# Kernel optimization log

Measured on AMD Instinct MI355X. Metric: run time of the kernel, lower is better.

The kernel has to match this reference:

```python
import jax, jax.numpy as jnp
import numpy as np

B, S, D, H, T, MAXLEN = 8, 1024, 768, 12, 384, 1024
HD = D // H  # spatial head dim = 64
SCALE = HD ** -0.5


def setup_inputs() -> dict:
    key = jax.random.key(0)
    ks = jax.random.split(key, 16)

    def lin(k, din, dout):
        kw, _ = jax.random.split(k)
        w = jax.random.normal(kw, (din, dout), jnp.float32) / np.sqrt(din).astype(np.float32)
        b = jnp.zeros((dout,), jnp.float32)
        return w, b

    Wqs, bqs = lin(ks[0], D, D)
    Wks, bks = lin(ks[1], D, D)
    Wvs, bvs = lin(ks[2], D, D)
    Wqt, bqt = lin(ks[3], T, D)
    Wkt, bkt = lin(ks[4], T, D)
    Wvt, bvt = lin(ks[5], T, D)
    Er = jax.random.normal(ks[6], (MAXLEN, HD), jnp.float32)
    patches = jax.random.normal(ks[7], (B, S, D), jnp.float32)
    time_emb = jax.random.normal(ks[8], (B, T), jnp.float32)
    return dict(patches=patches, time_emb=time_emb,
                Wqs=Wqs, bqs=bqs, Wks=Wks, bks=bks, Wvs=Wvs, bvs=bvs,
                Wqt=Wqt, bqt=bqt, Wkt=Wkt, bkt=bkt, Wvt=Wvt, bvt=bvt, Er=Er)


def _skew(QEr):
    # QEr: [B, H, S, S] -> pad one zero col on the left, reshape, drop first row.
    b, h, r, c = QEr.shape
    padded = jnp.pad(QEr, ((0, 0), (0, 0), (0, 0), (1, 0)))  # [B,H,r,c+1]
    reshaped = padded.reshape(b, h, c + 1, r)
    return reshaped[:, :, 1:, :]  # [B,H,S,S]


def reference(patches, time_emb, Wqs, bqs, Wks, bks, Wvs, bvs,
              Wqt, bqt, Wkt, bkt, Wvt, bvt, Er):
    b, s, _ = patches.shape

    def heads(x):  # [B,S,D] -> [B,H,S,HD]
        return x.reshape(b, -1, H, HD).transpose(0, 2, 1, 3)

    qs = heads(patches @ Wqs + bqs)
    ks = heads(patches @ Wks + bks)
    vs = heads(patches @ Wvs + bvs)
    qt = heads(time_emb @ Wqt + bqt)  # [B,H,1,HD]
    kt = heads(time_emb @ Wkt + bkt)
    vt = heads(time_emb @ Wvt + bvt)

    q = qs + qt
    k = ks + kt
    v = vs + vt

    Er_slice = Er[MAXLEN - s:, :]                      # [S, HD]
    QEr = jnp.einsum('bhsd,td->bhst', qs, Er_slice)    # [B,H,S,S]
    Srel = _skew(QEr)

    scores = (jnp.einsum('bhqd,bhkd->bhqk', q, k) + Srel) * SCALE
    attn = jax.nn.softmax(scores, axis=-1)
    out = jnp.einsum('bhqk,bhkd->bhqd', attn, v)       # [B,H,S,HD]
    return out.transpose(0, 2, 1, 3).reshape(b, s, H * HD)
```

## Files before the change

kernel.cpp:

```cpp
#include <hip/hip_runtime.h>

typedef __attribute__((ext_vector_type(8))) short short8;
typedef __attribute__((ext_vector_type(4))) float floatx4;

#define CSC 0.1803368801f

__device__ __forceinline__ unsigned short f2b(float f){
  unsigned int u = __builtin_bit_cast(unsigned int, f);
  unsigned int r = (u + 0x7fffu + ((u >> 16) & 1u)) >> 16;
  return (unsigned short)r;
}
__device__ __forceinline__ float b2f(unsigned short h){
  unsigned int u = ((unsigned int)h) << 16;
  return __builtin_bit_cast(float, u);
}
__device__ __forceinline__ floatx4 mfma16(short8 a, short8 b, floatx4 c){
  return __builtin_amdgcn_mfma_f32_16x16x32_bf16(a, b, c, 0, 0, 0);
}

__global__ __launch_bounds__(256) void transpose_w(
    const float* __restrict__ Wq, const float* __restrict__ Wk,
    const float* __restrict__ Wv, unsigned short* __restrict__ Wb){
  __shared__ float tile[64][65];
  int g = blockIdx.z;
  const float* W = (g==0) ? Wq : (g==1) ? Wk : Wv;
  int r0 = blockIdx.y*64, c0 = blockIdx.x*64;
  int tx = threadIdx.x & 63, ty = threadIdx.x >> 6;
  #pragma unroll
  for (int i=0;i<16;i++){
    int r = i*4 + ty;
    tile[r][tx] = W[(r0+r)*768 + c0 + tx];
  }
  __syncthreads();
  unsigned short* dst = Wb + g*589824;
  #pragma unroll
  for (int i=0;i<16;i++){
    int rr = i*4 + ty;
    dst[(c0+rr)*768 + r0 + tx] = f2b(tile[tx][rr]);
  }
}

__global__ __launch_bounds__(256) void convert_kernel(
    const float* __restrict__ patches, const float* __restrict__ Er,
    const float* __restrict__ temb,
    const float* __restrict__ Wqt, const float* __restrict__ bqt,
    const float* __restrict__ Wkt, const float* __restrict__ bkt,
    const float* __restrict__ Wvt, const float* __restrict__ bvt,
    unsigned short* __restrict__ Pb, unsigned short* __restrict__ Erb,
    float* __restrict__ Tmat){
  int blk = blockIdx.x, tid = threadIdx.x;
  if (blk < 3104){
    const float* src; unsigned short* dst; int idx;
    if (blk < 3072){ idx = blk*2048 + tid*8; src = patches; dst = Pb; }
    else           { idx = (blk-3072)*2048 + tid*8; src = Er; dst = Erb; }
    float4 f0 = *(const float4*)(src + idx);
    float4 f1 = *(const float4*)(src + idx + 4);
    uint4 pk;
    pk.x = (unsigned)f2b(f0.x) | ((unsigned)f2b(f0.y)<<16);
    pk.y = (unsigned)f2b(f0.z) | ((unsigned)f2b(f0.w)<<16);
    pk.z = (unsigned)f2b(f1.x) | ((unsigned)f2b(f1.y)<<16);
    pk.w = (unsigned)f2b(f1.z) | ((unsigned)f2b(f1.w)<<16);
    *(uint4*)(dst + idx) = pk;
  } else {
    int g = (blk-3104)>>3, bb = (blk-3104)&7;
    const float* Wt = (g==0)? Wqt : (g==1)? Wkt : Wvt;
    const float* bt = (g==0)? bqt : (g==1)? bkt : bvt;
    __shared__ float emb[384];
    for (int j=tid;j<384;j+=256) emb[j] = temb[bb*384 + j];
    __syncthreads();
    float acc0 = bt[tid], acc1 = bt[tid+256], acc2 = bt[tid+512];
    for (int t=0;t<384;t++){
      float e = emb[t];
      const float* wr = Wt + t*768;
      acc0 += e*wr[tid]; acc1 += e*wr[tid+256]; acc2 += e*wr[tid+512];
    }
    float* dst = Tmat + g*6144 + bb*768;
    float s = (g==0) ? CSC : 1.0f;
    dst[tid] = acc0*s; dst[tid+256] = acc1*s; dst[tid+512] = acc2*s;
  }
}

__global__ __launch_bounds__(256) void qkv_gemm(
    const unsigned short* __restrict__ Pb, const unsigned short* __restrict__ Wb,
    const float* __restrict__ bq, const float* __restrict__ bk,
    const float* __restrict__ bv, const float* __restrict__ Tmat,
    unsigned short* __restrict__ Qs, unsigned short* __restrict__ K,
    unsigned short* __restrict__ V){
  __shared__ unsigned short a_lds[128*72];
  __shared__ unsigned short b_lds[128*72];
  int g = blockIdx.z;
  int m0 = blockIdx.x*128, n0 = blockIdx.y*128;
  int tid = threadIdx.x, w = tid>>6, lane = tid&63, quad = lane>>4, l16 = lane&15;
  int wr = w>>1, wc = w&1;
  const unsigned short* Wg = Wb + g*589824;
  const float* bias = (g==0)? bq : (g==1)? bk : bv;
  floatx4 acc[4][4];
  #pragma unroll
  for (int i=0;i<4;i++)
    #pragma unroll
    for (int j=0;j<4;j++) acc[i][j] = (floatx4){0.f,0.f,0.f,0.f};

  for (int kt=0; kt<12; kt++){
    int k0 = kt*64;
    __syncthreads();
    #pragma unroll
    for (int i=0;i<4;i++){
      int idx = i*256 + tid;
      int r = idx >> 3, c = (idx & 7) << 3;
      *(uint4*)&a_lds[r*72 + c] = *(const uint4*)&Pb[(m0+r)*768 + k0 + c];
      *(uint4*)&b_lds[r*72 + c] = *(const uint4*)&Wg[(n0+r)*768 + k0 + c];
    }
    __syncthreads();
    #pragma unroll
    for (int ks=0; ks<2; ks++){
      short8 af[4], bf[4];
      #pragma unroll
      for (int mb=0;mb<4;mb++)
        af[mb] = *(const short8*)&a_lds[(wr*64+mb*16+l16)*72 + ks*32 + quad*8];
      #pragma unroll
      for (int nb=0;nb<4;nb++)
        bf[nb] = *(const short8*)&b_lds[(wc*64+nb*16+l16)*72 + ks*32 + quad*8];
      #pragma unroll
      for (int mb=0;mb<4;mb++)
        #pragma unroll
        for (int nb=0;nb<4;nb++)
          acc[mb][nb] = mfma16(af[mb], bf[nb], acc[mb][nb]);
    }
  }
  #pragma unroll
  for (int mb=0;mb<4;mb++)
  #pragma unroll
  for (int nb=0;nb<4;nb++)
  #pragma unroll
  for (int reg=0;reg<4;reg++){
    int m = m0 + wr*64 + mb*16 + quad*4 + reg;
    int n = n0 + wc*64 + nb*16 + l16;
    int bb = m >> 10, s = m & 1023, h = n >> 6, hd = n & 63;
    float v = acc[mb][nb][reg] + bias[n];
    int base = (bb*12 + h) << 16;
    if (g == 0){
      Qs[base + (s<<6) + hd] = f2b(v * CSC);
    } else {
      float tadd = Tmat[g*6144 + bb*768 + n];
      if (g == 1) K[base + (s<<6) + hd] = f2b(v + tadd);
      else        V[base + (hd<<10) + s] = f2b(v + tadd);
    }
  }
}

__global__ __launch_bounds__(256, 4) void attn_kernel(
    const unsigned short* __restrict__ Qsp, const unsigned short* __restrict__ Kp,
    const unsigned short* __restrict__ Vtp, const unsigned short* __restrict__ Erb,
    const float* __restrict__ Tq, float* __restrict__ out){
  __shared__ __align__(16) char smem[29696];
  unsigned short* k_lds  = (unsigned short*)smem;
  unsigned short* v_lds  = (unsigned short*)(smem + 9216);
  unsigned short* pw_all = (unsigned short*)(smem + 18432);

  int tid = threadIdx.x, w = tid>>6, lane = tid&63, quad = lane>>4, l16 = lane&15;
  unsigned short* pw = pw_all + w*1408;
  int q0 = blockIdx.x*64, h = blockIdx.y, b = blockIdx.z;
  int hb = (b*12 + h) << 16;
  const unsigned short* Qsh = Qsp + hb;
  const unsigned short* Kh  = Kp  + hb;
  const unsigned short* Vh  = Vtp + hb;
  const float* tqv = Tq + b*768 + h*64;

  int frow = w*16 + l16;
  int qrow = q0 + frow;
  int qrow1 = (qrow < 1023) ? qrow+1 : 1023;
  short8 qf[2], qlo[2], qhi[2];
  #pragma unroll
  for (int ks=0; ks<2; ks++){
    int c = ks*32 + quad*8;
    qlo[ks] = *(const short8*)&Qsh[(qrow <<6) + c];
    qhi[ks] = *(const short8*)&Qsh[(qrow1<<6) + c];
    float4 t0 = *(const float4*)&tqv[c];
    float4 t1 = *(const float4*)&tqv[c+4];
    short8 qq;
    qq[0]=(short)f2b(b2f((unsigned short)qlo[ks][0])+t0.x);
    qq[1]=(short)f2b(b2f((unsigned short)qlo[ks][1])+t0.y);
    qq[2]=(short)f2b(b2f((unsigned short)qlo[ks][2])+t0.z);
    qq[3]=(short)f2b(b2f((unsigned short)qlo[ks][3])+t0.w);
    qq[4]=(short)f2b(b2f((unsigned short)qlo[ks][4])+t1.x);
    qq[5]=(short)f2b(b2f((unsigned short)qlo[ks][5])+t1.y);
    qq[6]=(short)f2b(b2f((unsigned short)qlo[ks][6])+t1.z);
    qq[7]=(short)f2b(b2f((unsigned short)qlo[ks][7])+t1.w);
    qf[ks] = qq;
  }

  float lpart[4] = {0.f,0.f,0.f,0.f};
  floatx4 o_acc[4];
  #pragma unroll
  for (int ob=0;ob<4;ob++) o_acc[ob] = (floatx4){0.f,0.f,0.f,0.f};

  int ql = quad*4;
  int ub_lo = 3 - w;

  int sr = tid>>3, scc = (tid&7)<<3;
  uint4 kr0, kr1, vr0, vr1;
  kr0 = *(const uint4*)&Kh[(sr<<6) + scc];
  kr1 = *(const uint4*)&Kh[((sr+32)<<6) + scc];
  vr0 = *(const uint4*)&Vh[(sr<<10) + scc];
  vr1 = *(const uint4*)&Vh[((sr+32)<<10) + scc];

  for (int kt=0; kt<16; kt++){
    int k0 = kt*64, diag = k0 - q0;
    __syncthreads();
    *(uint4*)&k_lds[sr*72 + scc]      = kr0;
    *(uint4*)&k_lds[(sr+32)*72 + scc] = kr1;
    *(uint4*)&v_lds[sr*72 + scc]      = vr0;
    *(uint4*)&v_lds[(sr+32)*72 + scc] = vr1;
    __syncthreads();
    int k0n = (kt < 15) ? k0 + 64 : k0;
    kr0 = *(const uint4*)&Kh[((k0n+sr)<<6) + scc];
    kr1 = *(const uint4*)&Kh[((k0n+sr+32)<<6) + scc];
    vr0 = *(const uint4*)&Vh[(sr<<10) + k0n + scc];
    vr1 = *(const uint4*)&Vh[((sr+32)<<10) + k0n + scc];

    floatx4 sc[4];
    #pragma unroll
    for (int nb=0;nb<4;nb++){
      sc[nb] = (floatx4){0.f,0.f,0.f,0.f};
      #pragma unroll
      for (int ks=0;ks<2;ks++){
        short8 kf = *(const short8*)&k_lds[(nb*16+l16)*72 + ks*32 + quad*8];
        sc[nb] = mfma16(qf[ks], kf, sc[nb]);
      }
    }
    bool needL = (diag <= 0), needU = (diag >= 0);
    bool needSel = (diag == 0) || (diag == 64);
    for (int pass=0; pass<2; pass++){
      if ((pass==0 && !needL) || (pass==1 && !needU)) continue;
      int tbase = (pass==0) ? (960 + diag) : (diag - 65);
      const short8* af = (pass==0) ? qlo : qhi;
      #pragma unroll
      for (int lb=0; lb<5; lb++){
        int ub = ub_lo + lb;
        int t = tbase + ub*16 + l16;
        t = (t < 0) ? 0 : (t > 1023 ? 1023 : t);
        floatx4 pa = (floatx4){0.f,0.f,0.f,0.f};
        #pragma unroll
        for (int ks=0;ks<2;ks++){
          short8 ef = *(const short8*)&Erb[(t<<6) + ks*32 + quad*8];
          pa = mfma16(af[ks], ef, pa);
        }
        #pragma unroll
        for (int reg=0;reg<4;reg++)
          pw[(ql + reg)*88 + lb*16 + l16] = f2b(pa[reg]);
      }
      #pragma unroll
      for (int nb=0;nb<4;nb++)
      #pragma unroll
      for (int reg=0;reg<4;reg++){
        int qlr = ql + reg;
        int ki = nb*16 + l16;
        float bv = b2f(pw[qlr*88 + 15 + (nb*16 + l16) - qlr + (ub_lo - (3-w))*16]);
        if (needSel){
          int kq = diag + ki - (w*16 + qlr);
          bool sel = (pass==0) ? (kq <= 0) : (kq >= 2);
          bv = sel ? bv : 0.f;
        }
        sc[nb][reg] += bv;
      }
    }
    #pragma unroll
    for (int nb=0;nb<4;nb++)
    #pragma unroll
    for (int reg=0;reg<4;reg++){
      float p = __builtin_amdgcn_exp2f(sc[nb][reg]);
      lpart[reg] += p;
      pw[(ql + reg)*88 + nb*16 + l16] = f2b(p);
    }
    short8 pf[2];
    #pragma unroll
    for (int ks=0;ks<2;ks++)
      pf[ks] = *(const short8*)&pw[l16*88 + ks*32 + quad*8];
    #pragma unroll
    for (int ob=0;ob<4;ob++){
      #pragma unroll
      for (int ks=0;ks<2;ks++){
        short8 vf = *(const short8*)&v_lds[(ob*16+l16)*72 + ks*32 + quad*8];
        o_acc[ob] = mfma16(pf[ks], vf, o_acc[ob]);
      }
    }
  }
  float rl[4];
  #pragma unroll
  for (int reg=0;reg<4;reg++){
    float l = lpart[reg];
    #pragma unroll
    for (int off=1; off<16; off<<=1) l += __shfl_xor(l, off);
    rl[reg] = __builtin_amdgcn_rcpf(l);
  }
  #pragma unroll
  for (int ob=0;ob<4;ob++)
  #pragma unroll
  for (int reg=0;reg<4;reg++){
    int s = q0 + w*16 + quad*4 + reg;
    out[((b<<10) + s)*768 + (h<<6) + ob*16 + l16] = o_acc[ob][reg] * rl[reg];
  }
}

extern "C" void kernel_launch(void* const* d_in, const int* in_sizes, int n_in,
                              void* d_out, int out_size, void* d_ws, size_t ws_size,
                              hipStream_t stream) {
  const float* patches  = (const float*)d_in[0];
  const float* time_emb = (const float*)d_in[1];
  const float* Wqs = (const float*)d_in[2];  const float* bqs = (const float*)d_in[3];
  const float* Wks = (const float*)d_in[4];  const float* bks = (const float*)d_in[5];
  const float* Wvs = (const float*)d_in[6];  const float* bvs = (const float*)d_in[7];
  const float* Wqt = (const float*)d_in[8];  const float* bqt = (const float*)d_in[9];
  const float* Wkt = (const float*)d_in[10]; const float* bkt = (const float*)d_in[11];
  const float* Wvt = (const float*)d_in[12]; const float* bvt = (const float*)d_in[13];
  const float* Er  = (const float*)d_in[14];

  unsigned short* Qsp  = (unsigned short*)d_ws;
  unsigned short* Kp   = Qsp + 6291456;
  unsigned short* Vp   = Kp  + 6291456;
  unsigned short* Wbp  = Vp  + 6291456;
  unsigned short* Erbp = Wbp + 1769472;
  unsigned short* Pbp  = Erbp + 65536;
  float*          Tmat = (float*)(Pbp + 6291456);

  float* out = (float*)d_out;

  hipLaunchKernelGGL(convert_kernel, dim3(3128), dim3(256), 0, stream,
                     patches, Er, time_emb, Wqt, bqt, Wkt, bkt, Wvt, bvt,
                     Pbp, Erbp, Tmat);
  hipLaunchKernelGGL(transpose_w, dim3(12,12,3), dim3(256), 0, stream,
                     Wqs, Wks, Wvs, Wbp);
  hipLaunchKernelGGL(qkv_gemm, dim3(64,6,3), dim3(256), 0, stream,
                     Pbp, Wbp, bqs, bks, bvs, Tmat, Qsp, Kp, Vp);
  hipLaunchKernelGGL(attn_kernel, dim3(16,12,8), dim3(256), 0, stream,
                     Qsp, Kp, Vp, Erbp, Tmat, out);
}
```

Baseline: 374.4 us.

## Process two 64-row query sub-tiles per attention block to reuse K/V tiles

Each attention block now handles 128 query rows as two 64-row sub-tiles that share each K/V tile staged in LDS. This halves the grid and the global K/V loads and LDS staging per query row. In exchange it doubles accumulator and Q-fragment register use, which is why the launch-bounds occupancy hint drops from 4 to 3. It also serializes the relative-position and softmax work for the two sub-tiles through the same per-wave LDS scratch, and the smaller grid gives less parallelism.

Measured after the change: 360.4 us. 1.04x faster.

```diff
diff --git a/kernel.cpp b/kernel.cpp
--- a/kernel.cpp
+++ b/kernel.cpp
@@ -148,7 +148,7 @@
   }
 }
 
-__global__ __launch_bounds__(256, 4) void attn_kernel(
+__global__ __launch_bounds__(256, 3) void attn_kernel(
     const unsigned short* __restrict__ Qsp, const unsigned short* __restrict__ Kp,
     const unsigned short* __restrict__ Vtp, const unsigned short* __restrict__ Erb,
     const float* __restrict__ Tq, float* __restrict__ out){
@@ -159,7 +159,7 @@
 
   int tid = threadIdx.x, w = tid>>6, lane = tid&63, quad = lane>>4, l16 = lane&15;
   unsigned short* pw = pw_all + w*1408;
-  int q0 = blockIdx.x*64, h = blockIdx.y, b = blockIdx.z;
+  int q0 = blockIdx.x*128, h = blockIdx.y, b = blockIdx.z;
   int hb = (b*12 + h) << 16;
   const unsigned short* Qsh = Qsp + hb;
   const unsigned short* Kh  = Kp  + hb;
@@ -167,32 +167,37 @@
   const float* tqv = Tq + b*768 + h*64;
 
   int frow = w*16 + l16;
-  int qrow = q0 + frow;
-  int qrow1 = (qrow < 1023) ? qrow+1 : 1023;
-  short8 qf[2], qlo[2], qhi[2];
-  #pragma unroll
-  for (int ks=0; ks<2; ks++){
-    int c = ks*32 + quad*8;
-    qlo[ks] = *(const short8*)&Qsh[(qrow <<6) + c];
-    qhi[ks] = *(const short8*)&Qsh[(qrow1<<6) + c];
-    float4 t0 = *(const float4*)&tqv[c];
-    float4 t1 = *(const float4*)&tqv[c+4];
-    short8 qq;
-    qq[0]=(short)f2b(b2f((unsigned short)qlo[ks][0])+t0.x);
-    qq[1]=(short)f2b(b2f((unsigned short)qlo[ks][1])+t0.y);
-    qq[2]=(short)f2b(b2f((unsigned short)qlo[ks][2])+t0.z);
-    qq[3]=(short)f2b(b2f((unsigned short)qlo[ks][3])+t0.w);
-    qq[4]=(short)f2b(b2f((unsigned short)qlo[ks][4])+t1.x);
-    qq[5]=(short)f2b(b2f((unsigned short)qlo[ks][5])+t1.y);
-    qq[6]=(short)f2b(b2f((unsigned short)qlo[ks][6])+t1.z);
-    qq[7]=(short)f2b(b2f((unsigned short)qlo[ks][7])+t1.w);
-    qf[ks] = qq;
-  }
-
-  float lpart[4] = {0.f,0.f,0.f,0.f};
-  floatx4 o_acc[4];
-  #pragma unroll
-  for (int ob=0;ob<4;ob++) o_acc[ob] = (floatx4){0.f,0.f,0.f,0.f};
+  short8 qf[2][2], qlo[2][2], qhi[2][2];
+  #pragma unroll
+  for (int sub=0; sub<2; sub++){
+    int qrow = q0 + sub*64 + frow;
+    int qrow1 = (qrow < 1023) ? qrow+1 : 1023;
+    #pragma unroll
+    for (int ks=0; ks<2; ks++){
+      int c = ks*32 + quad*8;
+      qlo[sub][ks] = *(const short8*)&Qsh[(qrow <<6) + c];
+      qhi[sub][ks] = *(const short8*)&Qsh[(qrow1<<6) + c];
+      float4 t0 = *(const float4*)&tqv[c];
+      float4 t1 = *(const float4*)&tqv[c+4];
+      short8 qq;
+      qq[0]=(short)f2b(b2f((unsigned short)qlo[sub][ks][0])+t0.x);
+      qq[1]=(short)f2b(b2f((unsigned short)qlo[sub][ks][1])+t0.y);
+      qq[2]=(short)f2b(b2f((unsigned short)qlo[sub][ks][2])+t0.z);
+      qq[3]=(short)f2b(b2f((unsigned short)qlo[sub][ks][3])+t0.w);
+      qq[4]=(short)f2b(b2f((unsigned short)qlo[sub][ks][4])+t1.x);
+      qq[5]=(short)f2b(b2f((unsigned short)qlo[sub][ks][5])+t1.y);
+      qq[6]=(short)f2b(b2f((unsigned short)qlo[sub][ks][6])+t1.z);
+      qq[7]=(short)f2b(b2f((unsigned short)qlo[sub][ks][7])+t1.w);
+      qf[sub][ks] = qq;
+    }
+  }
+
+  float lpart[2][4] = {{0.f,0.f,0.f,0.f},{0.f,0.f,0.f,0.f}};
+  floatx4 o_acc[2][4];
+  #pragma unroll
+  for (int sub=0;sub<2;sub++)
+    #pragma unroll
+    for (int ob=0;ob<4;ob++) o_acc[sub][ob] = (floatx4){0.f,0.f,0.f,0.f};
 
   int ql = quad*4;
   int ub_lo = 3 - w;
@@ -205,7 +210,7 @@
   vr1 = *(const uint4*)&Vh[((sr+32)<<10) + scc];
 
   for (int kt=0; kt<16; kt++){
-    int k0 = kt*64, diag = k0 - q0;
+    int k0 = kt*64;
     __syncthreads();
     *(uint4*)&k_lds[sr*72 + scc]      = kr0;
     *(uint4*)&k_lds[(sr+32)*72 + scc] = kr1;
@@ -218,87 +223,97 @@
     vr0 = *(const uint4*)&Vh[(sr<<10) + k0n + scc];
     vr1 = *(const uint4*)&Vh[((sr+32)<<10) + k0n + scc];
 
-    floatx4 sc[4];
+    floatx4 sc[2][4];
     #pragma unroll
     for (int nb=0;nb<4;nb++){
-      sc[nb] = (floatx4){0.f,0.f,0.f,0.f};
+      sc[0][nb] = (floatx4){0.f,0.f,0.f,0.f};
+      sc[1][nb] = (floatx4){0.f,0.f,0.f,0.f};
       #pragma unroll
       for (int ks=0;ks<2;ks++){
         short8 kf = *(const short8*)&k_lds[(nb*16+l16)*72 + ks*32 + quad*8];
-        sc[nb] = mfma16(qf[ks], kf, sc[nb]);
+        sc[0][nb] = mfma16(qf[0][ks], kf, sc[0][nb]);
+        sc[1][nb] = mfma16(qf[1][ks], kf, sc[1][nb]);
       }
     }
-    bool needL = (diag <= 0), needU = (diag >= 0);
-    bool needSel = (diag == 0) || (diag == 64);
-    for (int pass=0; pass<2; pass++){
-      if ((pass==0 && !needL) || (pass==1 && !needU)) continue;
-      int tbase = (pass==0) ? (960 + diag) : (diag - 65);
-      const short8* af = (pass==0) ? qlo : qhi;
-      #pragma unroll
-      for (int lb=0; lb<5; lb++){
-        int ub = ub_lo + lb;
-        int t = tbase + ub*16 + l16;
-        t = (t < 0) ? 0 : (t > 1023 ? 1023 : t);
-        floatx4 pa = (floatx4){0.f,0.f,0.f,0.f};
+
+    #pragma unroll
+    for (int sub=0; sub<2; sub++){
+      int diag = k0 - q0 - sub*64;
+      bool needL = (diag <= 0), needU = (diag >= 0);
+      bool needSel = (diag == 0) || (diag == 64);
+      for (int pass=0; pass<2; pass++){
+        if ((pass==0 && !needL) || (pass==1 && !needU)) continue;
+        int tbase = (pass==0) ? (960 + diag) : (diag - 65);
+        const short8* af = (pass==0) ? qlo[sub] : qhi[sub];
+        #pragma unroll
+        for (int lb=0; lb<5; lb++){
+          int ub = ub_lo + lb;
+          int t = tbase + ub*16 + l16;
+          t = (t < 0) ? 0 : (t > 1023 ? 1023 : t);
+          floatx4 pa = (floatx4){0.f,0.f,0.f,0.f};
+          #pragma unroll
+          for (int ks=0;ks<2;ks++){
+            short8 ef = *(const short8*)&Erb[(t<<6) + ks*32 + quad*8];
+            pa = mfma16(af[ks], ef, pa);
+          }
+          #pragma unroll
+          for (int reg=0;reg<4;reg++)
+            pw[(ql + reg)*88 + lb*16 + l16] = f2b(pa[reg]);
+        }
+        #pragma unroll
+        for (int nb=0;nb<4;nb++)
+        #pragma unroll
+        for (int reg=0;reg<4;reg++){
+          int qlr = ql + reg;
+          int ki = nb*16 + l16;
+          float bv = b2f(pw[qlr*88 + 15 + ki - qlr]);
+          if (needSel){
+            int kq = diag + ki - (w*16 + qlr);
+            bool sel = (pass==0) ? (kq <= 0) : (kq >= 2);
+            bv = sel ? bv : 0.f;
+          }
+          sc[sub][nb][reg] += bv;
+        }
+      }
+      #pragma unroll
+      for (int nb=0;nb<4;nb++)
+      #pragma unroll
+      for (int reg=0;reg<4;reg++){
+        float p = __builtin_amdgcn_exp2f(sc[sub][nb][reg]);
+        lpart[sub][reg] += p;
+        pw[(ql + reg)*88 + nb*16 + l16] = f2b(p);
+      }
+      short8 pf[2];
+      #pragma unroll
+      for (int ks=0;ks<2;ks++)
+        pf[ks] = *(const short8*)&pw[l16*88 + ks*32 + quad*8];
+      #pragma unroll
+      for (int ob=0;ob<4;ob++){
         #pragma unroll
         for (int ks=0;ks<2;ks++){
-          short8 ef = *(const short8*)&Erb[(t<<6) + ks*32 + quad*8];
-          pa = mfma16(af[ks], ef, pa);
+          short8 vf = *(const short8*)&v_lds[(ob*16+l16)*72 + ks*32 + quad*8];
+          o_acc[sub][ob] = mfma16(pf[ks], vf, o_acc[sub][ob]);
         }
-        #pragma unroll
-        for (int reg=0;reg<4;reg++)
-          pw[(ql + reg)*88 + lb*16 + l16] = f2b(pa[reg]);
       }
-      #pragma unroll
-      for (int nb=0;nb<4;nb++)
-      #pragma unroll
-      for (int reg=0;reg<4;reg++){
-        int qlr = ql + reg;
-        int ki = nb*16 + l16;
-        float bv = b2f(pw[qlr*88 + 15 + (nb*16 + l16) - qlr + (ub_lo - (3-w))*16]);
-        if (needSel){
-          int kq = diag + ki - (w*16 + qlr);
-          bool sel = (pass==0) ? (kq <= 0) : (kq >= 2);
-          bv = sel ? bv : 0.f;
-        }
-        sc[nb][reg] += bv;
-      }
-    }
-    #pragma unroll
-    for (int nb=0;nb<4;nb++)
+    }
+  }
+  #pragma unroll
+  for (int sub=0;sub<2;sub++){
+    float rl[4];
     #pragma unroll
     for (int reg=0;reg<4;reg++){
-      float p = __builtin_amdgcn_exp2f(sc[nb][reg]);
-      lpart[reg] += p;
-      pw[(ql + reg)*88 + nb*16 + l16] = f2b(p);
-    }
-    short8 pf[2];
-    #pragma unroll
-    for (int ks=0;ks<2;ks++)
-      pf[ks] = *(const short8*)&pw[l16*88 + ks*32 + quad*8];
-    #pragma unroll
-    for (int ob=0;ob<4;ob++){
-      #pragma unroll
-      for (int ks=0;ks<2;ks++){
-        short8 vf = *(const short8*)&v_lds[(ob*16+l16)*72 + ks*32 + quad*8];
-        o_acc[ob] = mfma16(pf[ks], vf, o_acc[ob]);
-      }
-    }
-  }
-  float rl[4];
-  #pragma unroll
-  for (int reg=0;reg<4;reg++){
-    float l = lpart[reg];
-    #pragma unroll
-    for (int off=1; off<16; off<<=1) l += __shfl_xor(l, off);
-    rl[reg] = __builtin_amdgcn_rcpf(l);
-  }
-  #pragma unroll
-  for (int ob=0;ob<4;ob++)
-  #pragma unroll
-  for (int reg=0;reg<4;reg++){
-    int s = q0 + w*16 + quad*4 + reg;
-    out[((b<<10) + s)*768 + (h<<6) + ob*16 + l16] = o_acc[ob][reg] * rl[reg];
+      float l = lpart[sub][reg];
+      #pragma unroll
+      for (int off=1; off<16; off<<=1) l += __shfl_xor(l, off);
+      rl[reg] = __builtin_amdgcn_rcpf(l);
+    }
+    #pragma unroll
+    for (int ob=0;ob<4;ob++)
+    #pragma unroll
+    for (int reg=0;reg<4;reg++){
+      int s = q0 + sub*64 + w*16 + quad*4 + reg;
+      out[((b<<10) + s)*768 + (h<<6) + ob*16 + l16] = o_acc[sub][ob][reg] * rl[reg];
+    }
   }
 }
 
@@ -332,6 +347,6 @@
                      Wqs, Wks, Wvs, Wbp);
   hipLaunchKernelGGL(qkv_gemm, dim3(64,6,3), dim3(256), 0, stream,
                      Pbp, Wbp, bqs, bks, bvs, Tmat, Qsp, Kp, Vp);
-  hipLaunchKernelGGL(attn_kernel, dim3(16,12,8), dim3(256), 0, stream,
+  hipLaunchKernelGGL(attn_kernel, dim3(8,12,8), dim3(256), 0, stream,
                      Qsp, Kp, Vp, Erbp, Tmat, out);
 }
```

## Load K fragments directly from global and stage V transpose through LDS

Applied to the files above, without the earlier changes.

The attention kernel no longer stages K tiles in shared memory. Each wave loads its K MFMA fragments straight from global memory, which cuts LDS use from 29696 to 20480 bytes and removes the K LDS writes and reads. The QKV GEMM's V output path now transposes the tile through LDS and writes coalesced 16-byte chunks, replacing scattered 2-byte strided stores. The trade-off is that every wave issues its own K global loads, which are redundant across waves and no longer prefetched one tile ahead, so latency may be exposed.

Result: slower. 421.8 us (+12.7%).

```diff
diff --git a/kernel.cpp b/kernel.cpp
--- a/kernel.cpp
+++ b/kernel.cpp
@@ -86,8 +86,9 @@
     const float* __restrict__ bv, const float* __restrict__ Tmat,
     unsigned short* __restrict__ Qs, unsigned short* __restrict__ K,
     unsigned short* __restrict__ V){
-  __shared__ unsigned short a_lds[128*72];
-  __shared__ unsigned short b_lds[128*72];
+  __shared__ unsigned short smem_q[18432];
+  unsigned short* a_lds = smem_q;
+  unsigned short* b_lds = smem_q + 9216;
   int g = blockIdx.z;
   int m0 = blockIdx.x*128, n0 = blockIdx.y*128;
   int tid = threadIdx.x, w = tid>>6, lane = tid&63, quad = lane>>4, l16 = lane&15;
@@ -127,23 +128,49 @@
           acc[mb][nb] = mfma16(af[mb], bf[nb], acc[mb][nb]);
     }
   }
-  #pragma unroll
-  for (int mb=0;mb<4;mb++)
-  #pragma unroll
-  for (int nb=0;nb<4;nb++)
-  #pragma unroll
-  for (int reg=0;reg<4;reg++){
-    int m = m0 + wr*64 + mb*16 + quad*4 + reg;
-    int n = n0 + wc*64 + nb*16 + l16;
-    int bb = m >> 10, s = m & 1023, h = n >> 6, hd = n & 63;
-    float v = acc[mb][nb][reg] + bias[n];
-    int base = (bb*12 + h) << 16;
-    if (g == 0){
-      Qs[base + (s<<6) + hd] = f2b(v * CSC);
-    } else {
-      float tadd = Tmat[g*6144 + bb*768 + n];
-      if (g == 1) K[base + (s<<6) + hd] = f2b(v + tadd);
-      else        V[base + (hd<<10) + s] = f2b(v + tadd);
+  if (g < 2){
+    #pragma unroll
+    for (int mb=0;mb<4;mb++)
+    #pragma unroll
+    for (int nb=0;nb<4;nb++)
+    #pragma unroll
+    for (int reg=0;reg<4;reg++){
+      int m = m0 + wr*64 + mb*16 + quad*4 + reg;
+      int n = n0 + wc*64 + nb*16 + l16;
+      int bb = m >> 10, s = m & 1023, h = n >> 6, hd = n & 63;
+      float v = acc[mb][nb][reg] + bias[n];
+      int base = (bb*12 + h) << 16;
+      if (g == 0){
+        Qs[base + (s<<6) + hd] = f2b(v * CSC);
+      } else {
+        float tadd = Tmat[6144 + bb*768 + n];
+        K[base + (s<<6) + hd] = f2b(v + tadd);
+      }
+    }
+  } else {
+    __syncthreads();
+    int bb = m0 >> 10;
+    #pragma unroll
+    for (int mb=0;mb<4;mb++)
+    #pragma unroll
+    for (int nb=0;nb<4;nb++)
+    #pragma unroll
+    for (int reg=0;reg<4;reg++){
+      int ml = wr*64 + mb*16 + quad*4 + reg;
+      int nl = wc*64 + nb*16 + l16;
+      int n = n0 + nl;
+      float v = acc[mb][nb][reg] + bias[n] + Tmat[12288 + bb*768 + n];
+      smem_q[nl*136 + ml] = f2b(v);
+    }
+    __syncthreads();
+    int s0 = m0 & 1023;
+    #pragma unroll
+    for (int i=0;i<8;i++){
+      int idx = i*256 + tid;
+      int r = idx >> 4, c8 = (idx & 15) << 3;
+      int n = n0 + r, h = n >> 6, hd = n & 63;
+      int base = (bb*12 + h) << 16;
+      *(uint4*)&V[base + (hd<<10) + s0 + c8] = *(const uint4*)&smem_q[r*136 + c8];
     }
   }
 }
@@ -152,10 +179,9 @@
     const unsigned short* __restrict__ Qsp, const unsigned short* __restrict__ Kp,
     const unsigned short* __restrict__ Vtp, const unsigned short* __restrict__ Erb,
     const float* __restrict__ Tq, float* __restrict__ out){
-  __shared__ __align__(16) char smem[29696];
-  unsigned short* k_lds  = (unsigned short*)smem;
-  unsigned short* v_lds  = (unsigned short*)(smem + 9216);
-  unsigned short* pw_all = (unsigned short*)(smem + 18432);
+  __shared__ __align__(16) char smem[20480];
+  unsigned short* v_lds  = (unsigned short*)smem;
+  unsigned short* pw_all = (unsigned short*)(smem + 9216);
 
   int tid = threadIdx.x, w = tid>>6, lane = tid&63, quad = lane>>4, l16 = lane&15;
   unsigned short* pw = pw_all + w*1408;
@@ -198,23 +224,23 @@
   int ub_lo = 3 - w;
 
   int sr = tid>>3, scc = (tid&7)<<3;
-  uint4 kr0, kr1, vr0, vr1;
-  kr0 = *(const uint4*)&Kh[(sr<<6) + scc];
-  kr1 = *(const uint4*)&Kh[((sr+32)<<6) + scc];
+  uint4 vr0, vr1;
   vr0 = *(const uint4*)&Vh[(sr<<10) + scc];
   vr1 = *(const uint4*)&Vh[((sr+32)<<10) + scc];
 
   for (int kt=0; kt<16; kt++){
     int k0 = kt*64, diag = k0 - q0;
-    __syncthreads();
-    *(uint4*)&k_lds[sr*72 + scc]      = kr0;
-    *(uint4*)&k_lds[(sr+32)*72 + scc] = kr1;
+    short8 kf[4][2];
+    #pragma unroll
+    for (int nb=0;nb<4;nb++)
+      #pragma unroll
+      for (int ks=0;ks<2;ks++)
+        kf[nb][ks] = *(const short8*)&Kh[((k0+nb*16+l16)<<6) + ks*32 + quad*8];
+    __syncthreads();
     *(uint4*)&v_lds[sr*72 + scc]      = vr0;
     *(uint4*)&v_lds[(sr+32)*72 + scc] = vr1;
     __syncthreads();
     int k0n = (kt < 15) ? k0 + 64 : k0;
-    kr0 = *(const uint4*)&Kh[((k0n+sr)<<6) + scc];
-    kr1 = *(const uint4*)&Kh[((k0n+sr+32)<<6) + scc];
     vr0 = *(const uint4*)&Vh[(sr<<10) + k0n + scc];
     vr1 = *(const uint4*)&Vh[((sr+32)<<10) + k0n + scc];
 
@@ -223,10 +249,8 @@
     for (int nb=0;nb<4;nb++){
       sc[nb] = (floatx4){0.f,0.f,0.f,0.f};
       #pragma unroll
-      for (int ks=0;ks<2;ks++){
-        short8 kf = *(const short8*)&k_lds[(nb*16+l16)*72 + ks*32 + quad*8];
-        sc[nb] = mfma16(qf[ks], kf, sc[nb]);
-      }
+      for (int ks=0;ks<2;ks++)
+        sc[nb] = mfma16(qf[ks], kf[nb][ks], sc[nb]);
     }
     bool needL = (diag <= 0), needU = (diag >= 0);
     bool needSel = (diag == 0) || (diag == 64);
@@ -255,7 +279,7 @@
       for (int reg=0;reg<4;reg++){
         int qlr = ql + reg;
         int ki = nb*16 + l16;
-        float bv = b2f(pw[qlr*88 + 15 + (nb*16 + l16) - qlr + (ub_lo - (3-w))*16]);
+        float bv = b2f(pw[qlr*88 + 15 + ki - qlr]);
         if (needSel){
           int kq = diag + ki - (w*16 + qlr);
           bool sel = (pass==0) ? (kq <= 0) : (kq >= 2);
```
